# Kernel optimization log

Measured on AMD Instinct MI355X. Metric: run time of the kernel, lower is better.

## Reference

```python
import jax, jax.numpy as jnp
import numpy as np

N_NODES = 50000
N_EDGES = 800000
IN_CH, HID, LAT = 256, 128, 64


def setup_inputs() -> dict:
    key = jax.random.key(0)
    k1, k2, k3, k4 = jax.random.split(key, 4)
    x = jax.random.normal(k1, (N_NODES, IN_CH), dtype=jnp.float32)
    edge_index = jax.random.randint(k2, (2, N_EDGES), 0, N_NODES, dtype=jnp.int64)
    W1 = jax.random.normal(k3, (IN_CH, HID), dtype=jnp.float32) * (1.0 / np.sqrt(IN_CH))
    b1 = jnp.zeros((HID,), dtype=jnp.float32)
    W2 = jax.random.normal(k4, (HID, LAT), dtype=jnp.float32) * (1.0 / np.sqrt(HID))
    b2 = jnp.zeros((LAT,), dtype=jnp.float32)
    return {"x": x, "edge_index": edge_index, "W1": W1, "b1": b1, "W2": W2, "b2": b2}


def gcn_conv(x, src, dst, deg_inv_sqrt, W, b):
    # PyG GCNConv: h = x @ W; out[dst] += d_dst^-1/2 * d_src^-1/2 * h[src]; + bias
    h = x @ W                                   # [N, out]
    norm = deg_inv_sqrt[src] * deg_inv_sqrt[dst]  # [E+N]
    msg = h[src] * norm[:, None]                # [E+N, out] (gather + scale)
    out = jax.ops.segment_sum(msg, dst, num_segments=x.shape[0])
    return out + b


def reference(x, edge_index, W1, b1, W2, b2):
    n = x.shape[0]
    loop = jnp.arange(n, dtype=edge_index.dtype)
    # add self loops (GCNConv default)
    src = jnp.concatenate([edge_index[0], loop])
    dst = jnp.concatenate([edge_index[1], loop])
    deg = jax.ops.segment_sum(jnp.ones_like(dst, dtype=x.dtype), dst, num_segments=n)
    deg_inv_sqrt = jnp.where(deg > 0, jax.lax.rsqrt(deg), 0.0)
    h = jax.nn.relu(gcn_conv(x, src, dst, deg_inv_sqrt, W1, b1))
    h = jax.nn.relu(gcn_conv(h, src, dst, deg_inv_sqrt, W2, b2))
    return h
```

## Files before the change

### kernel.cpp

```cpp
#include <hip/hip_runtime.h>

#define N_NODES 50000
#define N_EDGES 800000
#define IN_CH 256
#define HID 128
#define LAT 64
#define CAP 64
#define NBIN 196
#define BINCAP 4864

typedef __attribute__((ext_vector_type(8))) short short8;
typedef __attribute__((ext_vector_type(16))) float f32x16;

static __device__ __forceinline__ unsigned short bf16_rne(float x) {
    unsigned u = __float_as_uint(x);
    unsigned r = (u + 0x7FFFu + ((u >> 16) & 1u)) >> 16;
    return (unsigned short)r;
}
static __device__ __forceinline__ float bf16_to_f(unsigned short h) {
    return __uint_as_float(((unsigned)h) << 16);
}

static __device__ __forceinline__ void add8(uint4 p, float* a) {
    a[0] += __uint_as_float(p.x << 16);
    a[1] += __uint_as_float(p.x & 0xFFFF0000u);
    a[2] += __uint_as_float(p.y << 16);
    a[3] += __uint_as_float(p.y & 0xFFFF0000u);
    a[4] += __uint_as_float(p.z << 16);
    a[5] += __uint_as_float(p.z & 0xFFFF0000u);
    a[6] += __uint_as_float(p.w << 16);
    a[7] += __uint_as_float(p.w & 0xFFFF0000u);
}
static __device__ __forceinline__ void fma8(uint4 p, float m, float* a) {
    a[0] = fmaf(m, __uint_as_float(p.x << 16), a[0]);
    a[1] = fmaf(m, __uint_as_float(p.x & 0xFFFF0000u), a[1]);
    a[2] = fmaf(m, __uint_as_float(p.y << 16), a[2]);
    a[3] = fmaf(m, __uint_as_float(p.y & 0xFFFF0000u), a[3]);
    a[4] = fmaf(m, __uint_as_float(p.z << 16), a[4]);
    a[5] = fmaf(m, __uint_as_float(p.z & 0xFFFF0000u), a[5]);
    a[6] = fmaf(m, __uint_as_float(p.w << 16), a[6]);
    a[7] = fmaf(m, __uint_as_float(p.w & 0xFFFF0000u), a[7]);
}

template <int K, int NN>
static __device__ __forceinline__ void split_store(const float* __restrict__ W,
                                                   unsigned short* __restrict__ Wf, int i) {
    constexpr int CT = NN / 32;
    int k = i / NN, n = i % NN;
    float w = W[i];
    unsigned short hi = bf16_rne(w);
    unsigned short lo = bf16_rne(w - bf16_to_f(hi));
    size_t off = ((size_t)((k >> 4) * CT + (n >> 5)) * 64 + ((n & 31) + 32 * ((k >> 3) & 1))) * 8 + (k & 7);
    Wf[off] = hi;
    Wf[(size_t)K * NN + off] = lo;
}

__global__ __launch_bounds__(256) void prep_kernel(const float* __restrict__ W1,
                                                   const float* __restrict__ W2,
                                                   int* __restrict__ binCnt,
                                                   unsigned short* __restrict__ W1f,
                                                   unsigned short* __restrict__ W2f) {
    int i = blockIdx.x * blockDim.x + threadIdx.x;
    if (i < NBIN) binCnt[i] = 0;
    if (i < IN_CH * HID) split_store<IN_CH, HID>(W1, W1f, i);
    if (i < HID * LAT) split_store<HID, LAT>(W2, W2f, i);
}

__global__ __launch_bounds__(256) void fill1_kernel(const int* __restrict__ ei,
                                                    int* __restrict__ binCnt,
                                                    unsigned int* __restrict__ binBuf, int E) {
    __shared__ int hist[NBIN];
    __shared__ int base[NBIN];
    const int tid = threadIdx.x;
    for (int i = tid; i < NBIN; i += 256) hist[i] = 0;
    __syncthreads();

    const int e0 = blockIdx.x * 2048 + tid;
    unsigned int pk[8];
    int bn[8], ofs[8];
#pragma unroll
    for (int i = 0; i < 8; ++i) {
        int e = e0 + 256 * i;
        bool v = e < E;
        int s = v ? ei[e] : 0;
        int d = v ? ei[E + e] : 0;
        bn[i] = d >> 8;
        pk[i] = (unsigned int)s | ((unsigned int)(d & 255) << 16);
        ofs[i] = v ? atomicAdd(&hist[bn[i]], 1) : -1;
    }
    __syncthreads();
    for (int i = tid; i < NBIN; i += 256)
        base[i] = hist[i] ? atomicAdd(&binCnt[i], hist[i]) : 0;
    __syncthreads();
#pragma unroll
    for (int i = 0; i < 8; ++i) {
        if (ofs[i] >= 0) {
            int p = base[bn[i]] + ofs[i];
            if (p < BINCAP) binBuf[(size_t)bn[i] * BINCAP + p] = pk[i];
        }
    }
}

__global__ __launch_bounds__(256) void fill2_kernel(const int* __restrict__ binCnt,
                                                    const unsigned int* __restrict__ binBuf,
                                                    int* __restrict__ cnt,
                                                    unsigned short* __restrict__ colb) {
    __shared__ int lcnt[256];
    const int b = blockIdx.x;
    const int tid = threadIdx.x;
    lcnt[tid] = 0;
    __syncthreads();
    int n = binCnt[b]; if (n > BINCAP) n = BINCAP;
    const int node0 = b << 8;
    for (int i = tid; i < n; i += 256) {
        unsigned int pk = binBuf[(size_t)b * BINCAP + i];
        int local = pk >> 16;
        int s = pk & 0xFFFF;
        int slot = atomicAdd(&lcnt[local], 1);
        if (slot < CAP) colb[(size_t)(node0 + local) * CAP + slot] = (unsigned short)s;
    }
    __syncthreads();
    int node = node0 + tid;
    if (node < N_NODES) cnt[node] = lcnt[tid];
}

template <int K, int NN, bool AFP32>
__global__ __launch_bounds__(256) void gemm_kernel(const void* __restrict__ Av,
                                                   const unsigned short* __restrict__ Wf,
                                                   const int* __restrict__ cnt,
                                                   unsigned short* __restrict__ C, int M) {
    constexpr int CT = NN / 32;
    constexpr int NT = (NN == 128) ? 2 : 1;
    __shared__ unsigned short As[4 * 512];
    __shared__ unsigned short Bs[2 * 2 * CT * 512];

    const int tid = threadIdx.x;
    const int lane = tid & 63;
    const int w = tid >> 6;
    const int row0 = blockIdx.x * 64;
    const int rt = w >> 1;
    const int ct0 = (NN == 128) ? ((w & 1) * 2) : (w & 1);

    f32x16 acc[NT];
#pragma unroll
    for (int nt = 0; nt < NT; ++nt)
#pragma unroll
        for (int q = 0; q < 16; ++q) acc[nt][q] = 0.0f;

    for (int kt = 0; kt < K; kt += 32) {
        {
            int m = tid >> 2, kc = tid & 3;
            int row = row0 + m; if (row >= M) row = M - 1;
            int s = kc >> 1, half = kc & 1, t = m >> 5;
            int ln = (m & 31) + 32 * half;
            uint4 v;
            if constexpr (AFP32) {
                const float* A = (const float*)Av;
                const float4 v0 = *(const float4*)(A + (size_t)row * K + kt + kc * 8);
                const float4 v1 = *(const float4*)(A + (size_t)row * K + kt + kc * 8 + 4);
                v.x = (unsigned)bf16_rne(v0.x) | ((unsigned)bf16_rne(v0.y) << 16);
                v.y = (unsigned)bf16_rne(v0.z) | ((unsigned)bf16_rne(v0.w) << 16);
                v.z = (unsigned)bf16_rne(v1.x) | ((unsigned)bf16_rne(v1.y) << 16);
                v.w = (unsigned)bf16_rne(v1.z) | ((unsigned)bf16_rne(v1.w) << 16);
            } else {
                const unsigned short* A = (const unsigned short*)Av;
                v = *(const uint4*)(A + (size_t)row * K + kt + kc * 8);
            }
            *(uint4*)&As[((s * 2 + t) << 9) + (ln << 3)] = v;
        }
        {
            const int sg0 = kt >> 4;
#pragma unroll
            for (int i0 = 0; i0 < CT * 256; i0 += 256) {
                int i = i0 + tid;
                int psl = i / (CT * 64), rem = i % (CT * 64);
                int p = psl >> 1, sl = psl & 1;
                const uint4* src = (const uint4*)(Wf + (size_t)p * K * NN + (size_t)(sg0 + sl) * CT * 512);
                ((uint4*)Bs)[i] = src[rem];
            }
        }
        __syncthreads();

#pragma unroll
        for (int sl = 0; sl < 2; ++sl) {
            short8 a = *(const short8*)&As[((sl * 2 + rt) << 9) + (lane << 3)];
            short8 bh[NT], bl[NT];
#pragma unroll
            for (int nt = 0; nt < NT; ++nt) {
                bh[nt] = *(const short8*)&Bs[((sl * CT + ct0 + nt) << 9) + (lane << 3)];
                bl[nt] = *(const short8*)&Bs[(((2 + sl) * CT + ct0 + nt) << 9) + (lane << 3)];
            }
#pragma unroll
            for (int nt = 0; nt < NT; ++nt) {
                acc[nt] = __builtin_amdgcn_mfma_f32_32x32x16_bf16(a, bh[nt], acc[nt], 0, 0, 0);
                acc[nt] = __builtin_amdgcn_mfma_f32_32x32x16_bf16(a, bl[nt], acc[nt], 0, 0, 0);
            }
        }
        __syncthreads();
    }

#pragma unroll
    for (int r = 0; r < 16; ++r) {
        int rowl = rt * 32 + (r & 3) + 8 * (r >> 2) + 4 * (lane >> 5);
        int row = row0 + rowl;
        if (row < M) {
            float sc = rsqrtf((float)cnt[row] + 1.0f);
#pragma unroll
            for (int nt = 0; nt < NT; ++nt) {
                int col = (ct0 + nt) * 32 + (lane & 31);
                C[(size_t)row * NN + col] = bf16_rne(acc[nt][r] * sc);
            }
        }
    }
}

template <int C, bool OBF16>
__global__ __launch_bounds__(256) void agg_kernel(const int* __restrict__ cnt,
                                                  const unsigned short* __restrict__ colb,
                                                  const unsigned short* __restrict__ hs,
                                                  const float* __restrict__ bias,
                                                  void* __restrict__ outv, int N) {
    constexpr int LPN = C / 8;
    constexpr int NPW = 64 / LPN;
    int node = (int)((blockIdx.x * blockDim.x + threadIdx.x) >> 6);
    int lane = threadIdx.x & 63;
    if (node >= N) return;
    const int g = lane / LPN;
    const int c = lane % LPN;

    int deg = cnt[node];
    int kk = deg < CAP ? deg : CAP;

    float acc[8];
#pragma unroll
    for (int q = 0; q < 8; ++q) acc[q] = 0.0f;
    if (g == 0) add8(*(const uint4*)(hs + (size_t)node * C + c * 8), acc);

    int myc = (lane < kk) ? (int)colb[(size_t)node * CAP + lane] : 0;

    int j = 0;
    for (; j + NPW * 4 <= kk; j += NPW * 4) {
        int s0 = __shfl(myc, j + g);
        int s1 = __shfl(myc, j + g + NPW);
        int s2 = __shfl(myc, j + g + 2 * NPW);
        int s3 = __shfl(myc, j + g + 3 * NPW);
        uint4 p0 = *(const uint4*)(hs + (size_t)s0 * C + c * 8);
        uint4 p1 = *(const uint4*)(hs + (size_t)s1 * C + c * 8);
        uint4 p2 = *(const uint4*)(hs + (size_t)s2 * C + c * 8);
        uint4 p3 = *(const uint4*)(hs + (size_t)s3 * C + c * 8);
        add8(p0, acc); add8(p1, acc); add8(p2, acc); add8(p3, acc);
    }
    if (j < kk) {
        bool v0 = (j + g) < kk, v1 = (j + g + NPW) < kk,
             v2 = (j + g + 2 * NPW) < kk, v3 = (j + g + 3 * NPW) < kk;
        int s0 = __shfl(myc, v0 ? (j + g) : 0);
        int s1 = __shfl(myc, v1 ? (j + g + NPW) : 0);
        int s2 = __shfl(myc, v2 ? (j + g + 2 * NPW) : 0);
        int s3 = __shfl(myc, v3 ? (j + g + 3 * NPW) : 0);
        uint4 p0 = *(const uint4*)(hs + (size_t)s0 * C + c * 8);
        uint4 p1 = *(const uint4*)(hs + (size_t)s1 * C + c * 8);
        uint4 p2 = *(const uint4*)(hs + (size_t)s2 * C + c * 8);
        uint4 p3 = *(const uint4*)(hs + (size_t)s3 * C + c * 8);
        fma8(p0, v0 ? 1.0f : 0.0f, acc);
        fma8(p1, v1 ? 1.0f : 0.0f, acc);
        fma8(p2, v2 ? 1.0f : 0.0f, acc);
        fma8(p3, v3 ? 1.0f : 0.0f, acc);
    }

#pragma unroll
    for (int s = LPN; s < 64; s <<= 1)
#pragma unroll
        for (int q = 0; q < 8; ++q) acc[q] += __shfl_xor(acc[q], s);

    if (lane < LPN) {
        float di = rsqrtf((float)deg + 1.0f);
        float o[8];
#pragma unroll
        for (int q = 0; q < 8; ++q)
            o[q] = fmaxf(fmaf(di, acc[q], bias[c * 8 + q]), 0.0f);
        if constexpr (OBF16) {
            unsigned short* out = (unsigned short*)outv;
            ushort4 lo4 = make_ushort4(bf16_rne(o[0]), bf16_rne(o[1]), bf16_rne(o[2]), bf16_rne(o[3]));
            ushort4 hi4 = make_ushort4(bf16_rne(o[4]), bf16_rne(o[5]), bf16_rne(o[6]), bf16_rne(o[7]));
            *(ushort4*)(out + (size_t)node * C + c * 8) = lo4;
            *(ushort4*)(out + (size_t)node * C + c * 8 + 4) = hi4;
        } else {
            float* out = (float*)outv;
            float4 o0 = {o[0], o[1], o[2], o[3]};
            float4 o1 = {o[4], o[5], o[6], o[7]};
            *(float4*)(out + (size_t)node * C + c * 8) = o0;
            *(float4*)(out + (size_t)node * C + c * 8 + 4) = o1;
        }
    }
}

extern "C" void kernel_launch(void* const* d_in, const int* in_sizes, int n_in,
                              void* d_out, int out_size, void* d_ws, size_t ws_size,
                              hipStream_t stream) {
    const float* x  = (const float*)d_in[0];
    const int*   ei = (const int*)d_in[1];
    const float* W1 = (const float*)d_in[2];
    const float* b1 = (const float*)d_in[3];
    const float* W2 = (const float*)d_in[4];
    const float* b2 = (const float*)d_in[5];

    const int N = N_NODES, E = N_EDGES;

    char* ws = (char*)d_ws;
    size_t off = 0;
    auto alloc = [&](size_t bytes) {
        void* p = ws + off;
        off = (off + bytes + 255) & ~(size_t)255;
        return p;
    };
    int*            cnt    = (int*)alloc((size_t)N * 4);
    unsigned short* colb   = (unsigned short*)alloc((size_t)N * CAP * 2);
    int*            binCnt = (int*)alloc((size_t)NBIN * 4);
    unsigned int*   binBuf = (unsigned int*)alloc((size_t)NBIN * BINCAP * 4);
    unsigned short* W1f    = (unsigned short*)alloc((size_t)2 * IN_CH * HID * 2);
    unsigned short* W2f    = (unsigned short*)alloc((size_t)2 * HID * LAT * 2);
    unsigned short* h1s    = (unsigned short*)alloc((size_t)N * HID * 2);
    unsigned short* act1   = (unsigned short*)alloc((size_t)N * HID * 2);
    unsigned short* h2s    = h1s;

    prep_kernel<<<(N + 255) / 256, 256, 0, stream>>>(W1, W2, binCnt, W1f, W2f);
    fill1_kernel<<<(E + 2047) / 2048, 256, 0, stream>>>(ei, binCnt, binBuf, E);
    fill2_kernel<<<NBIN, 256, 0, stream>>>(binCnt, binBuf, cnt, colb);

    gemm_kernel<IN_CH, HID, true><<<(N + 63) / 64, 256, 0, stream>>>(x, W1f, cnt, h1s, N);
    agg_kernel<HID, true><<<(N + 3) / 4, 256, 0, stream>>>(cnt, colb, h1s, b1, act1, N);

    gemm_kernel<HID, LAT, false><<<(N + 63) / 64, 256, 0, stream>>>(act1, W2f, cnt, h2s, N);
    agg_kernel<LAT, false><<<(N + 3) / 4, 256, 0, stream>>>(cnt, colb, h2s, b2, d_out, N);
}
```

Measured before the change: 199.1 us.

## Replace two-pass binned adjacency build with direct global-atomic fill

Swaps the two-kernel binning scheme (a shared-memory histogram into bins, then per-bin local slot assignment) for one kernel that does a global atomicAdd on each destination's count and writes the source straight into its slot. This removes one launch, the intermediate bin buffer and its extra read/write pass. In exchange there are 800K global atomics on random addresses and scattered 2-byte writes with poor coalescing, and the slot order within each node becomes nondeterministic. Zeroing of cnt moves into the prep kernel.

```diff
diff --git a/kernel.cpp b/kernel.cpp
--- a/kernel.cpp
+++ b/kernel.cpp
@@ -6,8 +6,6 @@
 #define HID 128
 #define LAT 64
 #define CAP 64
-#define NBIN 196
-#define BINCAP 4864
 
 typedef __attribute__((ext_vector_type(8))) short short8;
 typedef __attribute__((ext_vector_type(16))) float f32x16;
@@ -57,71 +55,24 @@
 
 __global__ __launch_bounds__(256) void prep_kernel(const float* __restrict__ W1,
                                                    const float* __restrict__ W2,
-                                                   int* __restrict__ binCnt,
+                                                   int* __restrict__ cnt,
                                                    unsigned short* __restrict__ W1f,
                                                    unsigned short* __restrict__ W2f) {
     int i = blockIdx.x * blockDim.x + threadIdx.x;
-    if (i < NBIN) binCnt[i] = 0;
+    if (i < N_NODES) cnt[i] = 0;
     if (i < IN_CH * HID) split_store<IN_CH, HID>(W1, W1f, i);
     if (i < HID * LAT) split_store<HID, LAT>(W2, W2f, i);
 }
 
-__global__ __launch_bounds__(256) void fill1_kernel(const int* __restrict__ ei,
-                                                    int* __restrict__ binCnt,
-                                                    unsigned int* __restrict__ binBuf, int E) {
-    __shared__ int hist[NBIN];
-    __shared__ int base[NBIN];
-    const int tid = threadIdx.x;
-    for (int i = tid; i < NBIN; i += 256) hist[i] = 0;
-    __syncthreads();
-
-    const int e0 = blockIdx.x * 2048 + tid;
-    unsigned int pk[8];
-    int bn[8], ofs[8];
-#pragma unroll
-    for (int i = 0; i < 8; ++i) {
-        int e = e0 + 256 * i;
-        bool v = e < E;
-        int s = v ? ei[e] : 0;
-        int d = v ? ei[E + e] : 0;
-        bn[i] = d >> 8;
-        pk[i] = (unsigned int)s | ((unsigned int)(d & 255) << 16);
-        ofs[i] = v ? atomicAdd(&hist[bn[i]], 1) : -1;
-    }
-    __syncthreads();
-    for (int i = tid; i < NBIN; i += 256)
-        base[i] = hist[i] ? atomicAdd(&binCnt[i], hist[i]) : 0;
-    __syncthreads();
-#pragma unroll
-    for (int i = 0; i < 8; ++i) {
-        if (ofs[i] >= 0) {
-            int p = base[bn[i]] + ofs[i];
-            if (p < BINCAP) binBuf[(size_t)bn[i] * BINCAP + p] = pk[i];
-        }
-    }
-}
-
-__global__ __launch_bounds__(256) void fill2_kernel(const int* __restrict__ binCnt,
-                                                    const unsigned int* __restrict__ binBuf,
-                                                    int* __restrict__ cnt,
-                                                    unsigned short* __restrict__ colb) {
-    __shared__ int lcnt[256];
-    const int b = blockIdx.x;
-    const int tid = threadIdx.x;
-    lcnt[tid] = 0;
-    __syncthreads();
-    int n = binCnt[b]; if (n > BINCAP) n = BINCAP;
-    const int node0 = b << 8;
-    for (int i = tid; i < n; i += 256) {
-        unsigned int pk = binBuf[(size_t)b * BINCAP + i];
-        int local = pk >> 16;
-        int s = pk & 0xFFFF;
-        int slot = atomicAdd(&lcnt[local], 1);
-        if (slot < CAP) colb[(size_t)(node0 + local) * CAP + slot] = (unsigned short)s;
-    }
-    __syncthreads();
-    int node = node0 + tid;
-    if (node < N_NODES) cnt[node] = lcnt[tid];
+__global__ __launch_bounds__(256) void fill_kernel(const int* __restrict__ ei,
+                                                   int* __restrict__ cnt,
+                                                   unsigned short* __restrict__ colb, int E) {
+    int e = blockIdx.x * 256 + threadIdx.x;
+    if (e >= E) return;
+    int s = ei[e];
+    int d = ei[E + e];
+    int slot = atomicAdd(&cnt[d], 1);
+    if (slot < CAP) colb[(size_t)d * CAP + slot] = (unsigned short)s;
 }
 
 template <int K, int NN, bool AFP32>
@@ -315,17 +266,14 @@
     };
     int*            cnt    = (int*)alloc((size_t)N * 4);
     unsigned short* colb   = (unsigned short*)alloc((size_t)N * CAP * 2);
-    int*            binCnt = (int*)alloc((size_t)NBIN * 4);
-    unsigned int*   binBuf = (unsigned int*)alloc((size_t)NBIN * BINCAP * 4);
     unsigned short* W1f    = (unsigned short*)alloc((size_t)2 * IN_CH * HID * 2);
     unsigned short* W2f    = (unsigned short*)alloc((size_t)2 * HID * LAT * 2);
     unsigned short* h1s    = (unsigned short*)alloc((size_t)N * HID * 2);
     unsigned short* act1   = (unsigned short*)alloc((size_t)N * HID * 2);
     unsigned short* h2s    = h1s;
 
-    prep_kernel<<<(N + 255) / 256, 256, 0, stream>>>(W1, W2, binCnt, W1f, W2f);
-    fill1_kernel<<<(E + 2047) / 2048, 256, 0, stream>>>(ei, binCnt, binBuf, E);
-    fill2_kernel<<<NBIN, 256, 0, stream>>>(binCnt, binBuf, cnt, colb);
+    prep_kernel<<<(N + 255) / 256, 256, 0, stream>>>(W1, W2, cnt, W1f, W2f);
+    fill_kernel<<<(E + 255) / 256, 256, 0, stream>>>(ei, cnt, colb, E);
 
     gemm_kernel<IN_CH, HID, true><<<(N + 63) / 64, 256, 0, stream>>>(x, W1f, cnt, h1s, N);
     agg_kernel<HID, true><<<(N + 3) / 4, 256, 0, stream>>>(cnt, colb, h1s, b1, act1, N);
```

Result: slower. 216.3 us (+8.7%).
